# Kernel tuning notes

Hardware: AMD Instinct MI355X
Metric: run time of the kernel (lower is better)

Reference implementation:

```python
import jax, jax.numpy as jnp
import numpy as np

B, T, D, H, W = 2, 8192, 512, 8, 256
d = D // H  # 64
NC = T // W  # number of chunks (T divisible by W)


def setup_inputs() -> dict:
    key = jax.random.key(0)
    ks = jax.random.split(key, 9)
    s = 1.0 / np.sqrt(D).astype(np.float32)
    x = jax.random.normal(ks[0], (B, T, D), jnp.float32)
    Wq = jax.random.normal(ks[1], (D, D), jnp.float32) * s
    Wk = jax.random.normal(ks[2], (D, D), jnp.float32) * s
    Wv = jax.random.normal(ks[3], (D, D), jnp.float32) * s
    Wo = jax.random.normal(ks[4], (D, D), jnp.float32) * s
    bq = jax.random.normal(ks[5], (D,), jnp.float32) * 0.01
    bk = jax.random.normal(ks[6], (D,), jnp.float32) * 0.01
    bv = jax.random.normal(ks[7], (D,), jnp.float32) * 0.01
    bo = jax.random.normal(ks[8], (D,), jnp.float32) * 0.01
    return {"x": x, "Wq": Wq, "bq": bq, "Wk": Wk, "bk": bk,
            "Wv": Wv, "bv": bv, "Wo": Wo, "bo": bo}


def _local_attention(q, k, v):
    # q, k, v: [B, H, T, d]. Each W-sized query chunk attends to keys in
    # [chunk_start - W, chunk_end + W) -> a 3W window, masked at boundaries.
    qc = q.reshape(B, H, NC, W, d)
    pad = ((0, 0), (0, 0), (W, W), (0, 0))
    kp = jnp.pad(k, pad)
    vp = jnp.pad(v, pad)
    # window gather indices into padded sequence: [NC, 3W]
    pos = jnp.arange(NC)[:, None] * W + jnp.arange(3 * W)[None, :]
    kw = kp[:, :, pos, :]  # [B, H, NC, 3W, d]
    vw = vp[:, :, pos, :]  # [B, H, NC, 3W, d]
    valid = (pos >= W) & (pos < T + W)  # [NC, 3W] true for real (unpadded) keys
    scores = jnp.einsum('bhcqd,bhckd->bhcqk', qc, kw) * (d ** -0.5)
    scores = jnp.where(valid[None, None, :, None, :], scores, -jnp.inf)
    attn = jax.nn.softmax(scores, axis=-1)
    out = jnp.einsum('bhcqk,bhckd->bhcqd', attn, vw)
    return out.reshape(B, H, T, d)


def reference(x, Wq, bq, Wk, bk, Wv, bv, Wo, bo):
    # Linear = x @ W.T + b (torch nn.Linear convention)
    q = (x @ Wq.T + bq).reshape(B, T, H, d).transpose(0, 2, 1, 3)
    # k_proj / v_proj run under torch.no_grad() in the original
    k = jax.lax.stop_gradient(x @ Wk.T + bk).reshape(B, T, H, d).transpose(0, 2, 1, 3)
    v = jax.lax.stop_gradient(x @ Wv.T + bv).reshape(B, T, H, d).transpose(0, 2, 1, 3)
    out = _local_attention(q, k, v)           # [B, H, T, d]
    out = out.transpose(0, 2, 1, 3).reshape(B, T, D)
    return out @ Wo.T + bo
```

## Files before the change

### kernel.cpp

```cpp
#include <hip/hip_runtime.h>
#include <hip/hip_bf16.h>

typedef unsigned short u16;
typedef unsigned int   u32;
typedef __bf16 bf16x8 __attribute__((ext_vector_type(8)));
typedef float  f32x4  __attribute__((ext_vector_type(4)));

#define BB 2
#define TT 8192
#define DD 512
#define HH 8
#define WW 256
#define DH 64
#define NX 8388608
#define NW 262144

__device__ __forceinline__ float b2f(u16 u) {
    unsigned int x = ((unsigned int)u) << 16;
    return __builtin_bit_cast(float, x);
}
__device__ __forceinline__ u16 f2b(float f) {
    __bf16 h = (__bf16)f;
    return __builtin_bit_cast(u16, h);
}
__device__ __forceinline__ bf16x8 ldsfrag(const u16* p) {
    return *(const bf16x8*)p;
}
__device__ __forceinline__ f32x4 mfma16(bf16x8 a, bf16x8 b, f32x4 c) {
    return __builtin_amdgcn_mfma_f32_16x16x32_bf16(a, b, c, 0, 0, 0);
}

typedef __attribute__((address_space(1))) u32 gu32;
typedef __attribute__((address_space(3))) u32 lu32;
__device__ __forceinline__ void gl_lds(const u16* g, u16* l) {
    __builtin_amdgcn_global_load_lds((gu32*)g, (lu32*)l, 16, 0, 0);
}

__device__ __forceinline__ void cvt8(const void* s, u16* d, long i, int f) {
    if (f) {
        const u32* sp = (const u32*)s + i;
        uint4 a = *(const uint4*)(sp);
        uint4 b = *(const uint4*)(sp + 4);
        u16 o[8];
        o[0] = f2b(__builtin_bit_cast(float, a.x));
        o[1] = f2b(__builtin_bit_cast(float, a.y));
        o[2] = f2b(__builtin_bit_cast(float, a.z));
        o[3] = f2b(__builtin_bit_cast(float, a.w));
        o[4] = f2b(__builtin_bit_cast(float, b.x));
        o[5] = f2b(__builtin_bit_cast(float, b.y));
        o[6] = f2b(__builtin_bit_cast(float, b.z));
        o[7] = f2b(__builtin_bit_cast(float, b.w));
        *(uint4*)(d + i) = *(const uint4*)o;
    } else {
        *(uint4*)(d + i) = *(const uint4*)((const u16*)s + i);
    }
}

__global__ void convert_all(const void* x, const void* Wq, const void* bq,
                            const void* Wk, const void* bk, const void* Wv,
                            const void* bv, const void* Wo, const void* bo,
                            u16* __restrict__ xb, u16* __restrict__ Wcat,
                            u16* __restrict__ Wob, u16* __restrict__ bcat,
                            u16* __restrict__ bob, int* __restrict__ flagw)
{
    __shared__ int sflag;
    const int tid = threadIdx.x;
    if (tid == 0) sflag = 0;
    __syncthreads();
    int mybad = 0;
    for (int i = tid; i < 2048; i += 256) {
        float v = b2f(((const u16*)x)[i]);
        if (!(fabsf(v) < 100.f)) mybad = 1;
    }
    if (mybad) atomicOr(&sflag, 1);
    __syncthreads();
    const int f = sflag ? 1 : 0;
    if (blockIdx.x == 0 && tid == 0) *flagw = f;

    long i = ((long)blockIdx.x * 256 + tid) * 8;
    if (i < NX)            { cvt8(x,  xb,           i, f); return; }
    i -= NX;
    if (i < NW)            { cvt8(Wq, Wcat,         i, f); return; }
    i -= NW;
    if (i < NW)            { cvt8(Wk, Wcat + NW,    i, f); return; }
    i -= NW;
    if (i < NW)            { cvt8(Wv, Wcat + 2*NW,  i, f); return; }
    i -= NW;
    if (i < NW)            { cvt8(Wo, Wob,          i, f); return; }
    i -= NW;
    if (i < 512)           { cvt8(bq, bcat,         i, f); return; }
    i -= 512;
    if (i < 512)           { cvt8(bk, bcat + 512,   i, f); return; }
    i -= 512;
    if (i < 512)           { cvt8(bv, bcat + 1024,  i, f); return; }
    i -= 512;
    if (i < 512)           { cvt8(bo, bob,          i, f); }
}

__global__ __launch_bounds__(512, 2)
void gemm256(const u16* __restrict__ A, const u16* __restrict__ Bw,
             const u16* __restrict__ bias, void* __restrict__ out0,
             u16* __restrict__ out1, u16* __restrict__ out2,
             int mode, const int* __restrict__ flagp)
{
    __shared__ __align__(16) u16 AsF[3][256 * 64];
    __shared__ __align__(16) u16 BsF[3][128 * 64];

    const int tid  = threadIdx.x;
    const int lane = tid & 63;
    const int wv   = tid >> 6;
    const int col  = lane & 15;
    const int quad = lane >> 4;
    const int wm   = (wv >> 1) * 64;
    const int wn   = (wv & 1) * 64;
    const int m0   = blockIdx.x * 256;
    const int n0   = blockIdx.y * 128;

    f32x4 acc[4][4] = {};

    const int lr  = lane >> 3;
    const int lc  = lane & 7;
    const int cbs = lc ^ lr;

    auto STG = [&](int buf, int k0, int half) {
        #pragma unroll
        for (int i = 0; i < 2; i++) {
            const int g = wv * 4 + half * 2 + i;
            gl_lds(A + (size_t)(m0 + g * 8 + lr) * 512 + k0 + cbs * 8,
                   &AsF[buf][g * 512]);
        }
        const int g2 = wv * 2 + half;
        gl_lds(Bw + (size_t)(n0 + g2 * 8 + lr) * 512 + k0 + cbs * 8,
               &BsF[buf][g2 * 512]);
    };

    auto PHASE = [&](int p, int kk, int q, int k2, int half, int dostage, int endw) {
        bf16x8 fa[4], fb[4];
        #pragma unroll
        for (int mi = 0; mi < 4; mi++)
            fa[mi] = ldsfrag(&AsF[p][(wm + mi * 16 + col) * 64 + ((kk * 4 + quad) ^ (col & 7)) * 8]);
        #pragma unroll
        for (int ni = 0; ni < 4; ni++)
            fb[ni] = ldsfrag(&BsF[p][(wn + ni * 16 + col) * 64 + ((kk * 4 + quad) ^ (col & 7)) * 8]);
        if (dostage) STG(q, k2, half);
        __builtin_amdgcn_s_barrier();
        asm volatile("s_waitcnt lgkmcnt(0)" ::: "memory");
        __builtin_amdgcn_sched_barrier(0);
        __builtin_amdgcn_s_setprio(1);
        #pragma unroll
        for (int mi = 0; mi < 4; mi++)
            #pragma unroll
            for (int ni = 0; ni < 4; ni++)
                acc[mi][ni] = mfma16(fa[mi], fb[ni], acc[mi][ni]);
        __builtin_amdgcn_s_setprio(0);
        if (endw == 6)      asm volatile("s_waitcnt vmcnt(6)" ::: "memory");
        else if (endw == 0) asm volatile("s_waitcnt vmcnt(0)" ::: "memory");
        __builtin_amdgcn_s_barrier();
        __builtin_amdgcn_sched_barrier(0);
    };

    STG(0, 0, 0);  STG(0, 0, 1);
    STG(1, 64, 0); STG(1, 64, 1);
    asm volatile("s_waitcnt vmcnt(6)" ::: "memory");
    __builtin_amdgcn_s_barrier();
    __builtin_amdgcn_sched_barrier(0);

    #pragma unroll
    for (int t = 0; t < 8; t++) {
        const int p  = t % 3;
        const int q  = (t + 2) % 3;
        const int k2 = (t + 2) * 64;
        const int st = (t < 6) ? 1 : 0;
        PHASE(p, 0, q, k2, 0, st, -1);
        PHASE(p, 1, q, k2, 1, st, (t < 6) ? 6 : ((t == 6) ? 0 : -1));
    }

    if (mode == 0) {
        #pragma unroll
        for (int ni = 0; ni < 4; ni++) {
            const int gn = n0 + wn + ni * 16 + col;
            const float bv = b2f(bias[gn]);
            const int seg = gn >> 9;
            #pragma unroll
            for (int mi = 0; mi < 4; mi++) {
                const int gmb = m0 + wm + mi * 16 + quad * 4;
                if (seg < 2) {
                    u16* dst = (seg == 0) ? (u16*)out0 : out1;
                    #pragma unroll
                    for (int r = 0; r < 4; r++)
                        dst[(size_t)(gmb + r) * 512 + (gn & 511)] = f2b(acc[mi][ni][r] + bv);
                } else {
                    const int d = gn & 63, hh = (gn >> 6) & 7;
                    const int bb = gmb >> 13, t = gmb & 8191;
                    u16 pb[4];
                    #pragma unroll
                    for (int r = 0; r < 4; r++) pb[r] = f2b(acc[mi][ni][r] + bv);
                    uint2 pk;
                    pk.x = pb[0] | ((u32)pb[1] << 16);
                    pk.y = pb[2] | ((u32)pb[3] << 16);
                    *(uint2*)&out2[((size_t)(bb * 8 + hh) * 64 + d) * 8192 + t] = pk;
                }
            }
        }
    } else {
        const int outf32 = *flagp;
        #pragma unroll
        for (int ni = 0; ni < 4; ni++) {
            const int gn = n0 + wn + ni * 16 + col;
            const float bv = b2f(bias[gn]);
            #pragma unroll
            for (int mi = 0; mi < 4; mi++) {
                #pragma unroll
                for (int r = 0; r < 4; r++) {
                    const int gm = m0 + wm + mi * 16 + quad * 4 + r;
                    const float v = acc[mi][ni][r] + bv;
                    if (outf32) ((float*)out0)[(size_t)gm * 512 + gn] = v;
                    else        ((u16*)out0)[(size_t)gm * 512 + gn]  = f2b(v);
                }
            }
        }
    }
}

#define PSW 72
__global__ __launch_bounds__(512, 4)
void attn_local(const u16* __restrict__ Qg, const u16* __restrict__ Kg,
                const u16* __restrict__ VTg, u16* __restrict__ Og)
{
    __shared__ __align__(16) u16 Ks[2][64 * 64];
    __shared__ __align__(16) u16 VTs[2][64 * 64];
    __shared__ __align__(16) u16 Ps[8][32 * PSW];

    const int tid  = threadIdx.x;
    const int lane = tid & 63;
    const int wv   = tid >> 6;
    const int col  = lane & 15;
    const int quad = lane >> 4;

    const int idx = blockIdx.x;
    const int c = idx & 31;
    const int h = (idx >> 5) & 7;
    const int b = idx >> 8;

    const int t0 = c * WW;
    const int wq = wv * 32;

    const int sc_lo = (c == 0) ? 4 : 0;
    const int nsc   = (c == 0 || c == 31) ? 8 : 12;

    const int ldr = lane >> 3;
    const int ldc = lane & 7;

    bf16x8 qf[2][2];
    {
        const size_t qbase = ((size_t)(b * TT + t0 + wq + col)) * DD + h * DH + quad * 8;
        #pragma unroll
        for (int qi = 0; qi < 2; qi++)
            #pragma unroll
            for (int kk = 0; kk < 2; kk++)
                qf[qi][kk] = *(const bf16x8*)(Qg + qbase + (size_t)qi * 16 * DD + kk * 32);
    }

    f32x4 o[4][2] = {};
    float lsum[2] = {0.f, 0.f};

    u16* psb = &Ps[wv][0];

    {
        const int kstart = t0 - WW + sc_lo * 64;
        const int rr = wv * 8 + ldr;
        const int cb = ldc ^ (rr & 7);
        gl_lds(Kg  + ((size_t)(b * TT + kstart + rr)) * DD + h * DH + cb * 8,
               &Ks[0][wv * 512]);
        gl_lds(VTg + ((size_t)((b * HH + h) * DH + rr)) * TT + kstart + cb * 8,
               &VTs[0][wv * 512]);
    }

    for (int it = 0; it < nsc; it++) {
        __syncthreads();
        if (it + 1 < nsc) {
            const int kstart = t0 - WW + (sc_lo + it + 1) * 64;
            const int buf = (it + 1) & 1;
            const int rr = wv * 8 + ldr;
            const int cb = ldc ^ (rr & 7);
            gl_lds(Kg  + ((size_t)(b * TT + kstart + rr)) * DD + h * DH + cb * 8,
                   &Ks[buf][wv * 512]);
            gl_lds(VTg + ((size_t)((b * HH + h) * DH + rr)) * TT + kstart + cb * 8,
                   &VTs[buf][wv * 512]);
        }
        const u16* ks = &Ks[it & 1][0];
        const u16* vs = &VTs[it & 1][0];

        f32x4 s[4][2];
        #pragma unroll
        for (int ns = 0; ns < 4; ns++)
            #pragma unroll
            for (int qi = 0; qi < 2; qi++)
                s[ns][qi] = (f32x4){0.f, 0.f, 0.f, 0.f};
        #pragma unroll
        for (int ns = 0; ns < 4; ns++) {
            const int row = ns * 16 + col;
            bf16x8 ka0 = ldsfrag(&ks[row * 64 + ((0 + quad) ^ (col & 7)) * 8]);
            bf16x8 ka1 = ldsfrag(&ks[row * 64 + ((4 + quad) ^ (col & 7)) * 8]);
            #pragma unroll
            for (int qi = 0; qi < 2; qi++) {
                s[ns][qi] = mfma16(ka0, qf[qi][0], s[ns][qi]);
                s[ns][qi] = mfma16(ka1, qf[qi][1], s[ns][qi]);
            }
        }

        #pragma unroll
        for (int ns = 0; ns < 4; ns++) {
            #pragma unroll
            for (int qi = 0; qi < 2; qi++) {
                u16 pb[4];
                #pragma unroll
                for (int r = 0; r < 4; r++) {
                    const float p = __expf(s[ns][qi][r] * 0.125f);
                    pb[r] = f2b(p);
                    lsum[qi] += p;
                }
                uint2 pk;
                pk.x = pb[0] | ((u32)pb[1] << 16);
                pk.y = pb[2] | ((u32)pb[3] << 16);
                *(uint2*)&psb[(qi * 16 + col) * PSW + ns * 16 + quad * 4] = pk;
            }
        }
        asm volatile("" ::: "memory");

        #pragma unroll
        for (int kt = 0; kt < 2; kt++) {
            bf16x8 pf[2];
            #pragma unroll
            for (int qi = 0; qi < 2; qi++)
                pf[qi] = ldsfrag(&psb[(qi * 16 + col) * PSW + kt * 32 + quad * 8]);
            #pragma unroll
            for (int di = 0; di < 4; di++) {
                bf16x8 va = ldsfrag(&vs[(di * 16 + col) * 64 + ((kt * 4 + quad) ^ (col & 7)) * 8]);
                #pragma unroll
                for (int qi = 0; qi < 2; qi++)
                    o[di][qi] = mfma16(va, pf[qi], o[di][qi]);
            }
        }
    }

    #pragma unroll
    for (int qi = 0; qi < 2; qi++) {
        float l = lsum[qi];
        l += __shfl_xor(l, 16);
        l += __shfl_xor(l, 32);
        lsum[qi] = 1.0f / l;
    }

    #pragma unroll
    for (int qi = 0; qi < 2; qi++) {
        const size_t ob = ((size_t)(b * TT + t0 + wq + qi * 16 + col)) * DD + h * DH + quad * 4;
        #pragma unroll
        for (int di = 0; di < 4; di++) {
            u16 pb[4];
            #pragma unroll
            for (int r = 0; r < 4; r++) pb[r] = f2b(o[di][qi][r] * lsum[qi]);
            uint2 pk;
            pk.x = pb[0] | ((u32)pb[1] << 16);
            pk.y = pb[2] | ((u32)pb[3] << 16);
            *(uint2*)&Og[ob + di * 16] = pk;
        }
    }
}

extern "C" void kernel_launch(void* const* d_in, const int* in_sizes, int n_in,
                              void* d_out, int out_size, void* d_ws, size_t ws_size,
                              hipStream_t stream)
{
    u16* ws   = (u16*)d_ws;
    u16* xb   = ws;
    u16* Wcat = xb + NX;
    u16* Wob  = Wcat + 3 * NW;
    u16* bcat = Wob + NW;
    u16* bob  = bcat + 1536;
    u16* qws  = bob + 512;
    u16* kws  = qws + NX;
    u16* vtws = kws + NX;
    u16* aws  = vtws + NX;
    int* flag = (int*)(aws + NX);

    convert_all<<<4609, 256, 0, stream>>>(
        d_in[0], d_in[1], d_in[2], d_in[3], d_in[4], d_in[5], d_in[6], d_in[7], d_in[8],
        xb, Wcat, Wob, bcat, bob, flag);

    gemm256<<<dim3(64, 12), 512, 0, stream>>>(xb, Wcat, bcat, qws, kws, vtws, 0, flag);
    attn_local<<<dim3(BB * HH * 32), 512, 0, stream>>>(qws, kws, vtws, aws);
    gemm256<<<dim3(64, 4), 512, 0, stream>>>(aws, Wob, bob, d_out, nullptr, nullptr, 1, flag);
}
```

Measured before the change: 193.0 us.

## Halve GEMM K-tile to 32 and raise occupancy to four blocks per CU

The 256x128 GEMM kernel now stages K-slices of 32 instead of 64 in its triple-buffered LDS ring. This cuts shared memory per block roughly in half, and launch bounds are raised so the compiler targets four resident blocks per CU instead of two. The swizzle, staging lambda and pipeline loop are rewritten to 16 iterations with one barrier pair per step. More resident blocks can hide latency, but the higher occupancy target limits registers per thread and could cause spills, and the extra barriers add synchronization.

```diff
diff --git a/kernel.cpp b/kernel.cpp
--- a/kernel.cpp
+++ b/kernel.cpp
@@ -97,14 +97,14 @@
     if (i < 512)           { cvt8(bo, bob,          i, f); }
 }
 
-__global__ __launch_bounds__(512, 2)
+__global__ __launch_bounds__(512, 4)
 void gemm256(const u16* __restrict__ A, const u16* __restrict__ Bw,
              const u16* __restrict__ bias, void* __restrict__ out0,
              u16* __restrict__ out1, u16* __restrict__ out2,
              int mode, const int* __restrict__ flagp)
 {
-    __shared__ __align__(16) u16 AsF[3][256 * 64];
-    __shared__ __align__(16) u16 BsF[3][128 * 64];
+    __shared__ __align__(16) u16 AsF[3][256 * 32];
+    __shared__ __align__(16) u16 BsF[3][128 * 32];
 
     const int tid  = threadIdx.x;
     const int lane = tid & 63;
@@ -118,34 +118,39 @@
 
     f32x4 acc[4][4] = {};
 
-    const int lr  = lane >> 3;
-    const int lc  = lane & 7;
-    const int cbs = lc ^ lr;
-
-    auto STG = [&](int buf, int k0, int half) {
+    const int sr  = lane >> 2;
+    const int cbs = (lane & 3) ^ (sr & 3);
+
+    auto STG = [&](int buf, int k0) {
         #pragma unroll
         for (int i = 0; i < 2; i++) {
-            const int g = wv * 4 + half * 2 + i;
-            gl_lds(A + (size_t)(m0 + g * 8 + lr) * 512 + k0 + cbs * 8,
+            const int g = wv * 2 + i;
+            gl_lds(A + (size_t)(m0 + g * 16 + sr) * 512 + k0 + cbs * 8,
                    &AsF[buf][g * 512]);
         }
-        const int g2 = wv * 2 + half;
-        gl_lds(Bw + (size_t)(n0 + g2 * 8 + lr) * 512 + k0 + cbs * 8,
-               &BsF[buf][g2 * 512]);
+        gl_lds(Bw + (size_t)(n0 + wv * 16 + sr) * 512 + k0 + cbs * 8,
+               &BsF[buf][wv * 512]);
     };
 
-    auto PHASE = [&](int p, int kk, int q, int k2, int half, int dostage, int endw) {
+    const int rdo = (quad ^ (col & 3)) * 8;
+
+    STG(0, 0);
+    STG(1, 32);
+    asm volatile("s_waitcnt vmcnt(3)" ::: "memory");
+    __builtin_amdgcn_s_barrier();
+    __builtin_amdgcn_sched_barrier(0);
+
+    #pragma unroll
+    for (int t = 0; t < 16; t++) {
+        const int p = t % 3;
         bf16x8 fa[4], fb[4];
         #pragma unroll
         for (int mi = 0; mi < 4; mi++)
-            fa[mi] = ldsfrag(&AsF[p][(wm + mi * 16 + col) * 64 + ((kk * 4 + quad) ^ (col & 7)) * 8]);
+            fa[mi] = ldsfrag(&AsF[p][(wm + mi * 16 + col) * 32 + rdo]);
         #pragma unroll
         for (int ni = 0; ni < 4; ni++)
-            fb[ni] = ldsfrag(&BsF[p][(wn + ni * 16 + col) * 64 + ((kk * 4 + quad) ^ (col & 7)) * 8]);
-        if (dostage) STG(q, k2, half);
-        __builtin_amdgcn_s_barrier();
-        asm volatile("s_waitcnt lgkmcnt(0)" ::: "memory");
-        __builtin_amdgcn_sched_barrier(0);
+            fb[ni] = ldsfrag(&BsF[p][(wn + ni * 16 + col) * 32 + rdo]);
+        if (t < 14) STG((t + 2) % 3, (t + 2) * 32);
         __builtin_amdgcn_s_setprio(1);
         #pragma unroll
         for (int mi = 0; mi < 4; mi++)
@@ -153,26 +158,15 @@
             for (int ni = 0; ni < 4; ni++)
                 acc[mi][ni] = mfma16(fa[mi], fb[ni], acc[mi][ni]);
         __builtin_amdgcn_s_setprio(0);
-        if (endw == 6)      asm volatile("s_waitcnt vmcnt(6)" ::: "memory");
-        else if (endw == 0) asm volatile("s_waitcnt vmcnt(0)" ::: "memory");
-        __builtin_amdgcn_s_barrier();
-        __builtin_amdgcn_sched_barrier(0);
-    };
-
-    STG(0, 0, 0);  STG(0, 0, 1);
-    STG(1, 64, 0); STG(1, 64, 1);
-    asm volatile("s_waitcnt vmcnt(6)" ::: "memory");
-    __builtin_amdgcn_s_barrier();
-    __builtin_amdgcn_sched_barrier(0);
-
-    #pragma unroll
-    for (int t = 0; t < 8; t++) {
-        const int p  = t % 3;
-        const int q  = (t + 2) % 3;
-        const int k2 = (t + 2) * 64;
-        const int st = (t < 6) ? 1 : 0;
-        PHASE(p, 0, q, k2, 0, st, -1);
-        PHASE(p, 1, q, k2, 1, st, (t < 6) ? 6 : ((t == 6) ? 0 : -1));
+        if (t < 14) {
+            asm volatile("s_waitcnt vmcnt(3)" ::: "memory");
+            __builtin_amdgcn_s_barrier();
+            __builtin_amdgcn_sched_barrier(0);
+        } else if (t == 14) {
+            asm volatile("s_waitcnt vmcnt(0)" ::: "memory");
+            __builtin_amdgcn_s_barrier();
+            __builtin_amdgcn_sched_barrier(0);
+        }
     }
 
     if (mode == 0) {
```

Measured after the change: 190.1 us. No clear change (-1.5%).
